# Optimization experiments

Hardware: AMD Instinct MI355X
Metric: run time of the kernel (lower is better)

## Reference

```python
import jax, jax.numpy as jnp
import numpy as np

B, T, C, H = 4, 2048, 1024, 16
D = C // H  # head dim = 64


def setup_inputs() -> dict:
    key = jax.random.key(0)
    ks = jax.random.split(key, 5)
    s = 1.0 / np.sqrt(C)
    return {
        "x": jax.random.normal(ks[0], (B, T, C), jnp.float32),
        "Wq": jax.random.normal(ks[1], (C, C), jnp.float32) * s,
        "bq": jnp.zeros((C,), jnp.float32),
        "Wk": jax.random.normal(ks[2], (C, C), jnp.float32) * s,
        "bk": jnp.zeros((C,), jnp.float32),
        "Wv": jax.random.normal(ks[3], (C, C), jnp.float32) * s,
        "bv": jnp.zeros((C,), jnp.float32),
        "Wp": jax.random.normal(ks[4], (C, C), jnp.float32) * s,
        "bp": jnp.zeros((C,), jnp.float32),
    }


def reference(x, Wq, bq, Wk, bk, Wv, bv, Wp, bp):
    # linear projections -> [B, H, T, D]
    def heads(t):
        return t.reshape(B, T, H, D).transpose(0, 2, 1, 3)
    q = heads(x @ Wq.T + bq)
    k = heads(x @ Wk.T + bk)
    v = heads(x @ Wv.T + bv)
    scale = 1.0 / np.sqrt(D)
    att = jnp.einsum("bhtd,bhsd->bhts", q, k) * scale  # [B,H,T,T]
    causal = jnp.tril(jnp.ones((T, T), bool))
    att = jnp.where(causal[None, None], att, -jnp.inf)
    att = jax.nn.softmax(att, axis=-1)
    y = jnp.einsum("bhts,bhsd->bhtd", att, v)  # [B,H,T,D]
    y = y.transpose(0, 2, 1, 3).reshape(B, T, C)
    return y @ Wp.T + bp
```

## Files before the change

### kernel.cpp

```cpp
#include <hip/hip_runtime.h>

typedef float f32x4 __attribute__((ext_vector_type(4)));
typedef float f32x16 __attribute__((ext_vector_type(16)));
typedef __bf16 bf16x8 __attribute__((ext_vector_type(8)));
typedef unsigned short u16x8 __attribute__((ext_vector_type(8)));
typedef unsigned int u32x4 __attribute__((ext_vector_type(4)));

#define SCQ 0.1803368801111183f

__device__ inline unsigned short f2bf(float f) {
  unsigned int u = __builtin_bit_cast(unsigned int, f);
  u += 0x7FFFu + ((u >> 16) & 1u);
  return (unsigned short)(u >> 16);
}

__device__ inline float fexp2(float x) {
#if __has_builtin(__builtin_amdgcn_exp2f)
  return __builtin_amdgcn_exp2f(x);
#else
  return exp2f(x);
#endif
}

__device__ inline unsigned int cvtpk_bf16(float a, float b) {
  unsigned int r;
  __asm__("v_cvt_pk_bf16_f32 %0, %1, %2" : "=v"(r) : "v"(a), "v"(b));
  return r;
}
__device__ inline void permswap32(unsigned int& a, unsigned int& b) {
  __asm__("v_permlane32_swap_b32 %0, %1" : "+v"(a), "+v"(b));
}

__device__ inline void gload_lds16(const unsigned short* g, unsigned short* l) {
  __builtin_amdgcn_global_load_lds(
      (const __attribute__((address_space(1))) unsigned int*)g,
      (__attribute__((address_space(3))) unsigned int*)l, 16, 0, 0);
}

__global__ void cvt_all(const float* __restrict__ x,
                        const float* __restrict__ wq, const float* __restrict__ wk,
                        const float* __restrict__ wv, const float* __restrict__ wp,
                        unsigned short* __restrict__ xb,
                        unsigned short* __restrict__ oq, unsigned short* __restrict__ ok,
                        unsigned short* __restrict__ ov, unsigned short* __restrict__ op_) {
  int gid = blockIdx.x;
  const float* src;
  unsigned short* dst;
  int i;
  if (gid < 8192) {
    src = x; dst = xb;
    i = (gid * 256 + threadIdx.x) * 4;
  } else {
    int g = gid - 8192;
    int m = g >> 10;
    src = (m == 0) ? wq : (m == 1) ? wk : (m == 2) ? wv : wp;
    dst = (m == 0) ? oq : (m == 1) ? ok : (m == 2) ? ov : op_;
    i = ((g & 1023) * 256 + threadIdx.x) * 4;
  }
  float4 f = *(const float4*)(src + i);
  ushort4 o;
  o.x = f2bf(f.x); o.y = f2bf(f.y); o.z = f2bf(f.z); o.w = f2bf(f.w);
  *(ushort4*)(dst + i) = o;
}

template <int MODE>
__global__ __launch_bounds__(256) void gemm128(const unsigned short* __restrict__ A,
                                               const unsigned short* __restrict__ Bt,
                                               const float* __restrict__ b0,
                                               const float* __restrict__ b1,
                                               const float* __restrict__ b2,
                                               void* __restrict__ out,
                                               unsigned short* __restrict__ vt,
                                               int M, int N, int K) {
  __shared__ __align__(16) unsigned short Sh[2][128 * 64];
  unsigned short* As = Sh[0];
  unsigned short* Bs = Sh[1];
  const int tid = threadIdx.x;
  const int lane = tid & 63, w = tid >> 6;
  const int l31 = lane & 31, half = lane >> 5;
  const int wm = w & 1, wn = w >> 1;
  const int m0 = blockIdx.x * 128, n0 = blockIdx.y * 128;

  f32x16 acc[2][2] = {};

  for (int kb = 0; kb < K; kb += 64) {
#pragma unroll
    for (int j = 0; j < 4; j++) {
      int ch = j * 256 + w * 64 + lane;
      int row = ch >> 3, pc = ch & 7;
      int c = pc ^ (row & 7);
      gload_lds16(A + (size_t)(m0 + row) * K + kb + c * 8, As + (size_t)(j * 256 + w * 64) * 8);
      gload_lds16(Bt + (size_t)(n0 + row) * K + kb + c * 8, Bs + (size_t)(j * 256 + w * 64) * 8);
    }
    __syncthreads();
#pragma unroll
    for (int ks = 0; ks < 64; ks += 16) {
      bf16x8 af[2], bfr[2];
#pragma unroll
      for (int at = 0; at < 2; at++) {
        int row = wm * 64 + at * 32 + l31;
        int pc = ((ks >> 3) + half) ^ (row & 7);
        af[at] = *(const bf16x8*)(As + row * 64 + pc * 8);
      }
#pragma unroll
      for (int nt = 0; nt < 2; nt++) {
        int row = wn * 64 + nt * 32 + l31;
        int pc = ((ks >> 3) + half) ^ (row & 7);
        bfr[nt] = *(const bf16x8*)(Bs + row * 64 + pc * 8);
      }
#pragma unroll
      for (int at = 0; at < 2; at++)
#pragma unroll
        for (int nt = 0; nt < 2; nt++)
          acc[at][nt] = __builtin_amdgcn_mfma_f32_32x32x16_bf16(af[at], bfr[nt], acc[at][nt], 0, 0, 0);
    }
    __syncthreads();
  }

  if (MODE == 0 && n0 >= 2048) {
    unsigned short* Lt = &Sh[0][0];
#pragma unroll
    for (int at = 0; at < 2; at++)
#pragma unroll
      for (int nt = 0; nt < 2; nt++) {
        int d = wn * 64 + nt * 32 + l31;
        float bv = b2[(n0 & 1023) + d];
        int swz = (d & 31) << 2;
#pragma unroll
        for (int reg = 0; reg < 16; reg++) {
          int t = wm * 64 + at * 32 + (reg & 3) + 8 * (reg >> 2) + 4 * half;
          Lt[d * 128 + (t ^ swz)] = f2bf(acc[at][nt][reg] + bv);
        }
      }
    __syncthreads();
    const int bb = m0 >> 11, t0 = m0 & 2047;
#pragma unroll
    for (int i = 0; i < 16; i++) {
      int d = (tid >> 5) + i * 8;
      int tb = (tid & 31) * 4;
      ushort4 val = *(const ushort4*)&Lt[d * 128 + (tb ^ ((d & 31) << 2))];
      int h = ((n0 & 1023) + d) >> 6;
      *(ushort4*)(vt + ((size_t)((bb * 16 + h) * 64 + (d & 63))) * 2048 + t0 + tb) = val;
    }
    return;
  }

#pragma unroll
  for (int at = 0; at < 2; at++)
#pragma unroll
    for (int nt = 0; nt < 2; nt++) {
      int col = n0 + wn * 64 + nt * 32 + l31;
      float bv, sc;
      int which = 0, cl = col;
      if (MODE == 0) {
        which = col >> 10; cl = col & 1023;
        const float* bp = (which == 0) ? b0 : b1;
        bv = bp[cl];
        sc = (which == 0) ? SCQ : 1.f;
      } else {
        bv = b0[col]; sc = 1.f;
      }
#pragma unroll
      for (int reg = 0; reg < 16; reg++) {
        int row = m0 + wm * 64 + at * 32 + (reg & 3) + 8 * (reg >> 2) + 4 * half;
        float v = (acc[at][nt][reg] + bv) * sc;
        if (MODE == 0) {
          int h = cl >> 6, d = cl & 63;
          int b = row >> 11, t = row & 2047;
          ((unsigned short*)out)[(size_t)which * 8388608 +
                                 ((size_t)((b * 16 + h) * 2048 + t)) * 64 + d] = f2bf(v);
        } else {
          ((float*)out)[(size_t)row * N + col] = v;
        }
      }
    }
}

template <int MODE>
__global__ __launch_bounds__(512, 2) void gemm8p(const unsigned short* __restrict__ A,
                                                 const unsigned short* __restrict__ Bt,
                                                 const float* __restrict__ b0,
                                                 const float* __restrict__ b1,
                                                 const float* __restrict__ b2,
                                                 void* __restrict__ out,
                                                 int M, int N, int K) {
  __shared__ __align__(16) unsigned short Lg[2][3][128 * 64];
  const int tid = threadIdx.x;
  const int lane = tid & 63, w = tid >> 6;
  const int qm = w >> 2, qn = w & 3;
  const int l15 = lane & 15, kq = lane >> 4;
  const int m0 = blockIdx.x * 128, n0 = blockIdx.y * 256;
  const int NT = K >> 6;

  const int row0 = tid >> 3, c0 = (tid & 7) ^ (row0 & 7);
  const int row1 = row0 + 64, c1 = (tid & 7) ^ (row1 & 7);

  auto stage = [&](int tt, int h) {
    if (tt < NT) {
      const unsigned short* s_ = (h == 0) ? A : Bt;
      const int rbase = (h == 0) ? m0 : (h == 1 ? n0 : n0 + 128);
      unsigned short* d = &Lg[tt & 1][h][0];
      gload_lds16(s_ + (size_t)(rbase + row0) * K + tt * 64 + c0 * 8, d + (size_t)tid * 8);
      gload_lds16(s_ + (size_t)(rbase + row1) * K + tt * 64 + c1 * 8, d + (size_t)(tid + 512) * 8);
    }
  };

  auto rdA = [&](const unsigned short* R, u16x8 (&a)[4][2]) {
#pragma unroll
    for (int mf = 0; mf < 4; mf++) {
      int row = qm * 64 + mf * 16 + l15;
#pragma unroll
      for (int kf = 0; kf < 2; kf++) {
        int pc = (kf * 4 + kq) ^ (row & 7);
        a[mf][kf] = *(const u16x8*)(R + row * 64 + pc * 8);
      }
    }
  };
  auto rdB = [&](const unsigned short* R, u16x8 (&bb)[2][2]) {
#pragma unroll
    for (int nf = 0; nf < 2; nf++) {
      int row = qn * 32 + nf * 16 + l15;
#pragma unroll
      for (int kf = 0; kf < 2; kf++) {
        int pc = (kf * 4 + kq) ^ (row & 7);
        bb[nf][kf] = *(const u16x8*)(R + row * 64 + pc * 8);
      }
    }
  };

  f32x4 acc[4][4] = {};

  auto domfma = [&](u16x8 (&a)[4][2], u16x8 (&bb)[2][2], int hb) {
#pragma unroll
    for (int mf = 0; mf < 4; mf++)
#pragma unroll
      for (int nf = 0; nf < 2; nf++)
#pragma unroll
        for (int kf = 0; kf < 2; kf++)
          acc[mf][hb * 2 + nf] = __builtin_amdgcn_mfma_f32_16x16x32_bf16(
              __builtin_bit_cast(bf16x8, a[mf][kf]),
              __builtin_bit_cast(bf16x8, bb[nf][kf]), acc[mf][hb * 2 + nf], 0, 0, 0);
  };

  stage(0, 0); stage(0, 1); stage(0, 2); stage(1, 0); stage(1, 1);
  __asm__ __volatile__("s_waitcnt vmcnt(4)" ::: "memory");
  __builtin_amdgcn_s_barrier();

  for (int tt = 0; tt < NT; ++tt) {
    const unsigned short* Ar  = &Lg[tt & 1][0][0];
    const unsigned short* B0r = &Lg[tt & 1][1][0];
    const unsigned short* B1r = &Lg[tt & 1][2][0];
    u16x8 aA[4][2], bb[2][2];

    rdA(Ar, aA); rdB(B0r, bb);
    stage(tt + 1, 2);
    __builtin_amdgcn_s_barrier();
    __asm__ __volatile__("s_waitcnt lgkmcnt(0)" ::: "memory");
    __builtin_amdgcn_sched_barrier(0);
    __builtin_amdgcn_s_setprio(1);
    domfma(aA, bb, 0);
    __builtin_amdgcn_s_setprio(0);
    __builtin_amdgcn_s_barrier();

    rdB(B1r, bb);
    stage(tt + 2, 0); stage(tt + 2, 1);
    __builtin_amdgcn_s_barrier();
    __asm__ __volatile__("s_waitcnt lgkmcnt(0)" ::: "memory");
    __builtin_amdgcn_sched_barrier(0);
    __builtin_amdgcn_s_setprio(1);
    domfma(aA, bb, 1);
    __builtin_amdgcn_s_setprio(0);
    if (tt < NT - 2) {
      __asm__ __volatile__("s_waitcnt vmcnt(4)" ::: "memory");
    } else if (tt == NT - 2) {
      __asm__ __volatile__("s_waitcnt vmcnt(0)" ::: "memory");
    }
    __builtin_amdgcn_s_barrier();
  }

#pragma unroll
  for (int nfg = 0; nfg < 4; nfg++) {
    const int col = n0 + (nfg >> 1) * 128 + qn * 32 + (nfg & 1) * 16 + l15;
    float bv = b0[col];
#pragma unroll
    for (int mf = 0; mf < 4; mf++) {
      f32x4 v4 = acc[mf][nfg];
#pragma unroll
      for (int r = 0; r < 4; r++) {
        int row = m0 + qm * 64 + mf * 16 + kq * 4 + r;
        ((float*)out)[(size_t)row * N + col] = v4[r] + bv;
      }
    }
  }
}

__global__ __launch_bounds__(256, 2) void attn_kernel(const unsigned short* __restrict__ Q,
                                                      const unsigned short* __restrict__ Km,
                                                      const unsigned short* __restrict__ Vt,
                                                      unsigned short* __restrict__ Y) {
  constexpr int T = 2048, D = 64;
  __shared__ __align__(16) unsigned short Ks[2][64 * 64];
  __shared__ __align__(16) unsigned short Vs[2][64 * 64];
  const int tid = threadIdx.x;
  const int lane = tid & 63, w = tid >> 6;
  const int l31 = lane & 31, half = lane >> 5;
  const int bh = blockIdx.x;
  const int b = bh >> 4, h = bh & 15;
  const int p = blockIdx.y;
  const unsigned short* Qp = Q + (size_t)bh * T * D;
  const unsigned short* Kp = Km + (size_t)bh * T * D;
  const unsigned short* Vp = Vt + (size_t)bh * D * T;

  const int bch0 = (w * 2) * 64, bch1 = (w * 2 + 1) * 64;
  const int ch0 = bch0 + lane, ch1 = bch1 + lane;
  const int row0 = ch0 >> 3, c0 = (ch0 & 7) ^ (row0 & 7);
  const int row1 = ch1 >> 3, c1 = (ch1 & 7) ^ (row1 & 7);

  for (int phase = 0; phase < 2; ++phase) {
    const int jt = phase ? (63 - (p * 4 + w)) : (p * 4 + w);
    const int qt = jt * 32;
    const int nit = phase ? (32 - 2 * p) : (2 * p + 2);
    const int qg = qt + l31;

    bf16x8 aq[4];
#pragma unroll
    for (int kc = 0; kc < 4; kc++)
      aq[kc] = *(const bf16x8*)(Qp + (size_t)qg * D + kc * 16 + half * 8);
    __asm__ __volatile__("" :: "v"(__builtin_bit_cast(f32x4, aq[0])),
                              "v"(__builtin_bit_cast(f32x4, aq[1])),
                              "v"(__builtin_bit_cast(f32x4, aq[2])),
                              "v"(__builtin_bit_cast(f32x4, aq[3])));

    f32x16 o0 = {}, o1 = {};
    float lsum = 0.f;

    gload_lds16(Kp + (size_t)row0 * 64 + c0 * 8, Ks[0] + bch0 * 8);
    gload_lds16(Kp + (size_t)row1 * 64 + c1 * 8, Ks[0] + bch1 * 8);
    gload_lds16(Vp + (size_t)row0 * T + c0 * 8, Vs[0] + bch0 * 8);
    gload_lds16(Vp + (size_t)row1 * T + c1 * 8, Vs[0] + bch1 * 8);

    int cur = 0;
    for (int it = 0; it < nit; ++it) {
      const int s0 = it * 64;
      if (it + 1 < nit) {
        const int s1 = s0 + 64;
        unsigned short* kd = Ks[cur ^ 1];
        unsigned short* vd = Vs[cur ^ 1];
        gload_lds16(Kp + (size_t)(s1 + row0) * 64 + c0 * 8, kd + bch0 * 8);
        gload_lds16(Kp + (size_t)(s1 + row1) * 64 + c1 * 8, kd + bch1 * 8);
        gload_lds16(Vp + (size_t)row0 * T + s1 + c0 * 8, vd + bch0 * 8);
        gload_lds16(Vp + (size_t)row1 * T + s1 + c1 * 8, vd + bch1 * 8);
        __asm__ __volatile__("s_waitcnt vmcnt(4)" ::: "memory");
      } else {
        __asm__ __volatile__("s_waitcnt vmcnt(0)" ::: "memory");
      }
      __builtin_amdgcn_s_barrier();
      __builtin_amdgcn_sched_barrier(0);

      if (s0 <= qt + 31) {
        const unsigned short* Kb_ = Ks[cur];
        const unsigned short* Vb_ = Vs[cur];

        f32x16 sacc0 = {}, sacc1 = {};
#pragma unroll
        for (int kc = 0; kc < 4; kc++) {
          int kr0 = l31;
          int cc0 = (kc * 2 + half) ^ (kr0 & 7);
          u16x8 k0 = *(const u16x8*)(Kb_ + kr0 * 64 + cc0 * 8);
          sacc0 = __builtin_amdgcn_mfma_f32_32x32x16_bf16(
              __builtin_bit_cast(bf16x8, k0), aq[kc], sacc0, 0, 0, 0);
          int kr1 = 32 + l31;
          int cc1 = (kc * 2 + half) ^ (kr1 & 7);
          u16x8 k1 = *(const u16x8*)(Kb_ + kr1 * 64 + cc1 * 8);
          sacc1 = __builtin_amdgcn_mfma_f32_32x32x16_bf16(
              __builtin_bit_cast(bf16x8, k1), aq[kc], sacc1, 0, 0, 0);
        }

        const bool full = (s0 + 63) <= qt;
        float e0_[16], e1_[16];
        if (full) {
#pragma unroll
          for (int r = 0; r < 16; r++) { e0_[r] = fexp2(sacc0[r]); lsum += e0_[r]; }
#pragma unroll
          for (int r = 0; r < 16; r++) { e1_[r] = fexp2(sacc1[r]); lsum += e1_[r]; }
        } else {
#pragma unroll
          for (int r = 0; r < 16; r++) {
            int sg = s0 + (r & 3) + 8 * (r >> 2) + 4 * half;
            float ex = fexp2(sacc0[r]);
            ex = (sg > qg) ? 0.f : ex;
            e0_[r] = ex; lsum += ex;
          }
#pragma unroll
          for (int r = 0; r < 16; r++) {
            int sg = s0 + 32 + (r & 3) + 8 * (r >> 2) + 4 * half;
            float ex = fexp2(sacc1[r]);
            ex = (sg > qg) ? 0.f : ex;
            e1_[r] = ex; lsum += ex;
          }
        }

        bf16x8 pf[4];
        auto pack2 = [&](const float* e_, int kbase) {
#pragma unroll
          for (int kl = 0; kl < 2; kl++) {
            int base = kl * 8;
            unsigned int a0 = cvtpk_bf16(e_[base + 0], e_[base + 1]);
            unsigned int b0v = cvtpk_bf16(e_[base + 4], e_[base + 5]);
            permswap32(a0, b0v);
            unsigned int a1 = cvtpk_bf16(e_[base + 2], e_[base + 3]);
            unsigned int b1v = cvtpk_bf16(e_[base + 6], e_[base + 7]);
            permswap32(a1, b1v);
            u32x4 t = {a0, a1, b0v, b1v};
            pf[kbase + kl] = __builtin_bit_cast(bf16x8, t);
          }
        };
        pack2(e0_, 0);
        pack2(e1_, 2);

#pragma unroll
        for (int kc = 0; kc < 4; kc++) {
          int vr0 = l31;
          int cc0 = (kc * 2 + half) ^ (vr0 & 7);
          u16x8 v0 = *(const u16x8*)(Vb_ + vr0 * 64 + cc0 * 8);
          o0 = __builtin_amdgcn_mfma_f32_32x32x16_bf16(
              __builtin_bit_cast(bf16x8, v0), pf[kc], o0, 0, 0, 0);
          int vr1 = 32 + l31;
          int cc1 = (kc * 2 + half) ^ (vr1 & 7);
          u16x8 v1 = *(const u16x8*)(Vb_ + vr1 * 64 + cc1 * 8);
          o1 = __builtin_amdgcn_mfma_f32_32x32x16_bf16(
              __builtin_bit_cast(bf16x8, v1), pf[kc], o1, 0, 0, 0);
        }
      }

      __builtin_amdgcn_sched_barrier(0);
      __builtin_amdgcn_s_barrier();
      cur ^= 1;
    }

    float tot = lsum + __shfl_xor(lsum, 32);
    float inv = 1.f / tot;
    unsigned short* Yrow = Y + ((size_t)(b * T + qg)) * 1024 + h * 64;
#pragma unroll
    for (int rp = 0; rp < 8; rp++) {
      int r = rp * 2;
      int d = (r & 3) + 8 * (r >> 2) + 4 * half;
      *(unsigned int*)(Yrow + d)      = cvtpk_bf16(o0[r] * inv, o0[r + 1] * inv);
      *(unsigned int*)(Yrow + 32 + d) = cvtpk_bf16(o1[r] * inv, o1[r + 1] * inv);
    }
  }
}

extern "C" void kernel_launch(void* const* d_in, const int* in_sizes, int n_in,
                              void* d_out, int out_size, void* d_ws, size_t ws_size,
                              hipStream_t stream) {
  const float* x  = (const float*)d_in[0];
  const float* Wq = (const float*)d_in[1];
  const float* bq = (const float*)d_in[2];
  const float* Wk = (const float*)d_in[3];
  const float* bk = (const float*)d_in[4];
  const float* Wv = (const float*)d_in[5];
  const float* bv = (const float*)d_in[6];
  const float* Wp = (const float*)d_in[7];
  const float* bp = (const float*)d_in[8];

  char* ws = (char*)d_ws;
  unsigned short* xb  = (unsigned short*)(ws + 0);
  unsigned short* wqb = (unsigned short*)(ws + 16777216);
  unsigned short* wkb = (unsigned short*)(ws + 18874368);
  unsigned short* wvb = (unsigned short*)(ws + 20971520);
  unsigned short* wpb = (unsigned short*)(ws + 23068672);
  unsigned short* Qb  = (unsigned short*)(ws + 25165824);
  unsigned short* Kb  = (unsigned short*)(ws + 41943040);
  unsigned short* Vtb = (unsigned short*)(ws + 58720256);
  unsigned short* Yb  = xb;

  cvt_all<<<12288, 256, 0, stream>>>(x, Wq, Wk, Wv, Wp, xb, wqb, wkb, wvb, wpb);

  gemm128<0><<<dim3(64, 24), 256, 0, stream>>>(xb, wqb, bq, bk, bv, Qb, Vtb, 8192, 3072, 1024);

  attn_kernel<<<dim3(64, 8), 256, 0, stream>>>(Qb, Kb, Vtb, Yb);

  gemm8p<1><<<dim3(64, 4), 512, 0, stream>>>(Yb, wpb, bp, bp, bp, d_out, 8192, 1024, 1024);
}
```

Before: 236.8 us.

## Replace QKV GEMM with 256x256-tile 8-wave pipelined kernel

The 128x128 single-buffered QKV projection GEMM is replaced with a 256x256-tile, 512-thread kernel. It double-buffers LDS through async global-to-LDS loads staged in quarter-tiles and interleaves LDS reads, prefetch and 16x16x32 MFMA phases with barriers and s_setprio. The aim is more operand reuse per tile and load latency hidden behind MFMA work. The V-transpose epilogue is reworked for the larger tile. In exchange it uses more LDS (128KB per block) and registers, and launches fewer blocks (384 instead of 1536), which could leave CUs underfilled.

Result: no change. 241.2 us (+1.9%).

```diff
diff --git a/kernel.cpp b/kernel.cpp
--- a/kernel.cpp
+++ b/kernel.cpp
@@ -63,125 +63,205 @@
   *(ushort4*)(dst + i) = o;
 }
 
-template <int MODE>
-__global__ __launch_bounds__(256) void gemm128(const unsigned short* __restrict__ A,
-                                               const unsigned short* __restrict__ Bt,
-                                               const float* __restrict__ b0,
-                                               const float* __restrict__ b1,
-                                               const float* __restrict__ b2,
-                                               void* __restrict__ out,
-                                               unsigned short* __restrict__ vt,
-                                               int M, int N, int K) {
-  __shared__ __align__(16) unsigned short Sh[2][128 * 64];
-  unsigned short* As = Sh[0];
-  unsigned short* Bs = Sh[1];
+__global__ __launch_bounds__(512, 2) void gemm256qkv(const unsigned short* __restrict__ A,
+                                                     const unsigned short* __restrict__ Bt,
+                                                     const float* __restrict__ b0,
+                                                     const float* __restrict__ b1,
+                                                     const float* __restrict__ b2,
+                                                     unsigned short* __restrict__ out,
+                                                     unsigned short* __restrict__ vt,
+                                                     int K) {
+  __shared__ __align__(16) unsigned short Lg[2][4][128 * 64];
   const int tid = threadIdx.x;
   const int lane = tid & 63, w = tid >> 6;
-  const int l31 = lane & 31, half = lane >> 5;
-  const int wm = w & 1, wn = w >> 1;
-  const int m0 = blockIdx.x * 128, n0 = blockIdx.y * 128;
-
-  f32x16 acc[2][2] = {};
-
-  for (int kb = 0; kb < K; kb += 64) {
-#pragma unroll
-    for (int j = 0; j < 4; j++) {
-      int ch = j * 256 + w * 64 + lane;
-      int row = ch >> 3, pc = ch & 7;
-      int c = pc ^ (row & 7);
-      gload_lds16(A + (size_t)(m0 + row) * K + kb + c * 8, As + (size_t)(j * 256 + w * 64) * 8);
-      gload_lds16(Bt + (size_t)(n0 + row) * K + kb + c * 8, Bs + (size_t)(j * 256 + w * 64) * 8);
-    }
-    __syncthreads();
-#pragma unroll
-    for (int ks = 0; ks < 64; ks += 16) {
-      bf16x8 af[2], bfr[2];
-#pragma unroll
-      for (int at = 0; at < 2; at++) {
-        int row = wm * 64 + at * 32 + l31;
-        int pc = ((ks >> 3) + half) ^ (row & 7);
-        af[at] = *(const bf16x8*)(As + row * 64 + pc * 8);
-      }
-#pragma unroll
-      for (int nt = 0; nt < 2; nt++) {
-        int row = wn * 64 + nt * 32 + l31;
-        int pc = ((ks >> 3) + half) ^ (row & 7);
-        bfr[nt] = *(const bf16x8*)(Bs + row * 64 + pc * 8);
-      }
-#pragma unroll
-      for (int at = 0; at < 2; at++)
-#pragma unroll
-        for (int nt = 0; nt < 2; nt++)
-          acc[at][nt] = __builtin_amdgcn_mfma_f32_32x32x16_bf16(af[at], bfr[nt], acc[at][nt], 0, 0, 0);
-    }
-    __syncthreads();
-  }
-
-  if (MODE == 0 && n0 >= 2048) {
-    unsigned short* Lt = &Sh[0][0];
-#pragma unroll
-    for (int at = 0; at < 2; at++)
-#pragma unroll
-      for (int nt = 0; nt < 2; nt++) {
-        int d = wn * 64 + nt * 32 + l31;
-        float bv = b2[(n0 & 1023) + d];
-        int swz = (d & 31) << 2;
-#pragma unroll
-        for (int reg = 0; reg < 16; reg++) {
-          int t = wm * 64 + at * 32 + (reg & 3) + 8 * (reg >> 2) + 4 * half;
-          Lt[d * 128 + (t ^ swz)] = f2bf(acc[at][nt][reg] + bv);
+  const int qm = w >> 2, qn = w & 3;
+  const int l15 = lane & 15, kq = lane >> 4;
+
+  const int wg = blockIdx.x;
+  const int bm = wg & 31, bn = wg >> 5;
+  const int m0 = bm * 256, n0 = bn * 256;
+  const int NT = K >> 6, NT4 = NT << 2;
+
+  const int row0 = tid >> 3, c0 = (tid & 7) ^ (row0 & 7);
+  const int row1 = row0 + 64, c1 = (tid & 7) ^ (row1 & 7);
+  const int ch0 = tid, ch1 = tid + 512;
+
+  auto stage = [&](int g) {
+    if (g < NT4) {
+      const int tt = g >> 2, h = g & 3;
+      const unsigned short* s_;
+      int rbase, reg_;
+      if (h == 0)      { s_ = A;  rbase = m0;       reg_ = 0; }
+      else if (h == 3) { s_ = A;  rbase = m0 + 128; reg_ = 1; }
+      else if (h == 1) { s_ = Bt; rbase = n0;       reg_ = 2; }
+      else             { s_ = Bt; rbase = n0 + 128; reg_ = 3; }
+      unsigned short* d = &Lg[tt & 1][reg_][0];
+      gload_lds16(s_ + (size_t)(rbase + row0) * K + tt * 64 + c0 * 8, d + ch0 * 8);
+      gload_lds16(s_ + (size_t)(rbase + row1) * K + tt * 64 + c1 * 8, d + ch1 * 8);
+    }
+  };
+
+  auto rdAh = [&](const unsigned short* R, u16x8 (&a)[4][2]) {
+#pragma unroll
+    for (int mf = 0; mf < 4; mf++) {
+      int row = qm * 64 + mf * 16 + l15;
+#pragma unroll
+      for (int kf = 0; kf < 2; kf++) {
+        int pc = (kf * 4 + kq) ^ (row & 7);
+        a[mf][kf] = *(const u16x8*)(R + row * 64 + pc * 8);
+      }
+    }
+  };
+  auto rdBh = [&](const unsigned short* R, u16x8 (&bb)[2][2]) {
+#pragma unroll
+    for (int nf = 0; nf < 2; nf++) {
+      int row = qn * 32 + nf * 16 + l15;
+#pragma unroll
+      for (int kf = 0; kf < 2; kf++) {
+        int pc = (kf * 4 + kq) ^ (row & 7);
+        bb[nf][kf] = *(const u16x8*)(R + row * 64 + pc * 8);
+      }
+    }
+  };
+  auto domfma = [&](u16x8 (&a)[4][2], u16x8 (&bb)[2][2], f32x4 (*ac)[2]) {
+#pragma unroll
+    for (int mf = 0; mf < 4; mf++)
+#pragma unroll
+      for (int nf = 0; nf < 2; nf++)
+#pragma unroll
+        for (int kf = 0; kf < 2; kf++)
+          ac[mf][nf] = __builtin_amdgcn_mfma_f32_16x16x32_bf16(
+              __builtin_bit_cast(bf16x8, a[mf][kf]),
+              __builtin_bit_cast(bf16x8, bb[nf][kf]), ac[mf][nf], 0, 0, 0);
+  };
+
+  f32x4 acc[4][4][2] = {};
+
+#pragma unroll
+  for (int g = 0; g < 7; ++g) stage(g);
+  __asm__ __volatile__("s_waitcnt vmcnt(6)" ::: "memory");
+  __builtin_amdgcn_s_barrier();
+
+  for (int tt = 0; tt < NT; ++tt) {
+    const unsigned short* A0r = &Lg[tt & 1][0][0];
+    const unsigned short* A1r = &Lg[tt & 1][1][0];
+    const unsigned short* B0r = &Lg[tt & 1][2][0];
+    const unsigned short* B1r = &Lg[tt & 1][3][0];
+    const int gb = 7 + 4 * tt;
+    u16x8 aA[4][2], bb0[2][2], bb1[2][2];
+
+    rdAh(A0r, aA); rdBh(B0r, bb0);
+    stage(gb + 0);
+    __builtin_amdgcn_s_barrier();
+    __asm__ __volatile__("s_waitcnt lgkmcnt(0)" ::: "memory");
+    __builtin_amdgcn_sched_barrier(0);
+    __builtin_amdgcn_s_setprio(1);
+    domfma(aA, bb0, acc[0]);
+    __builtin_amdgcn_s_setprio(0);
+    __builtin_amdgcn_s_barrier();
+
+    rdBh(B1r, bb1);
+    stage(gb + 1);
+    __builtin_amdgcn_s_barrier();
+    __asm__ __volatile__("s_waitcnt lgkmcnt(0)" ::: "memory");
+    __builtin_amdgcn_sched_barrier(0);
+    __builtin_amdgcn_s_setprio(1);
+    domfma(aA, bb1, acc[1]);
+    __builtin_amdgcn_s_setprio(0);
+    __builtin_amdgcn_s_barrier();
+
+    rdAh(A1r, aA);
+    stage(gb + 2);
+    __builtin_amdgcn_s_barrier();
+    __asm__ __volatile__("s_waitcnt lgkmcnt(0)" ::: "memory");
+    __builtin_amdgcn_sched_barrier(0);
+    __builtin_amdgcn_s_setprio(1);
+    domfma(aA, bb0, acc[2]);
+    __builtin_amdgcn_s_setprio(0);
+    __builtin_amdgcn_s_barrier();
+
+    stage(gb + 3);
+    __builtin_amdgcn_s_setprio(1);
+    domfma(aA, bb1, acc[3]);
+    __builtin_amdgcn_s_setprio(0);
+    if (tt < NT - 2) {
+      __asm__ __volatile__("s_waitcnt vmcnt(6)" ::: "memory");
+    } else if (tt == NT - 2) {
+      __asm__ __volatile__("s_waitcnt vmcnt(0)" ::: "memory");
+    }
+    __builtin_amdgcn_s_barrier();
+  }
+
+  if (n0 >= 2048) {
+    unsigned short* Ld = &Lg[0][0][0];
+    const int bb_ = m0 >> 11, t0g = m0 & 2047;
+    const int vbase = n0 - 2048;
+#pragma unroll
+    for (int dh = 0; dh < 2; dh++) {
+      if (dh) __syncthreads();
+#pragma unroll
+      for (int ph = 0; ph < 2; ph++) {
+        const int p = ph * 2 + dh;
+#pragma unroll
+        for (int nf = 0; nf < 2; nf++) {
+          const int dl = qn * 32 + nf * 16 + l15;
+          const float bv = b2[vbase + dh * 128 + dl];
+          const int swz = (dl & 31) << 2;
+#pragma unroll
+          for (int mf = 0; mf < 4; mf++) {
+            f32x4 v4 = acc[p][mf][nf];
+#pragma unroll
+            for (int rp = 0; rp < 2; rp++) {
+              const int tl = ph * 128 + qm * 64 + mf * 16 + kq * 4 + rp * 2;
+              unsigned int pk = cvtpk_bf16(v4[rp * 2] + bv, v4[rp * 2 + 1] + bv);
+              *(unsigned int*)&Ld[dl * 256 + (tl ^ swz)] = pk;
+            }
+          }
         }
       }
-    __syncthreads();
-    const int bb = m0 >> 11, t0 = m0 & 2047;
-#pragma unroll
-    for (int i = 0; i < 16; i++) {
-      int d = (tid >> 5) + i * 8;
-      int tb = (tid & 31) * 4;
-      ushort4 val = *(const ushort4*)&Lt[d * 128 + (tb ^ ((d & 31) << 2))];
-      int h = ((n0 & 1023) + d) >> 6;
-      *(ushort4*)(vt + ((size_t)((bb * 16 + h) * 64 + (d & 63))) * 2048 + t0 + tb) = val;
+      __syncthreads();
+#pragma unroll
+      for (int i = 0; i < 16; i++) {
+        const int d = (tid >> 5) + (i & 7) * 16;
+        const int tb = (tid & 31) * 4 + (i >> 3) * 128;
+        ushort4 val = *(const ushort4*)&Ld[d * 256 + (tb ^ ((d & 31) << 2))];
+        const int cl = vbase + dh * 128 + d;
+        const int hh = cl >> 6, dd = cl & 63;
+        *(ushort4*)(vt + ((size_t)((bb_ * 16 + hh) * 64 + dd)) * 2048 + t0g + tb) = val;
+      }
     }
     return;
   }
 
 #pragma unroll
-  for (int at = 0; at < 2; at++)
-#pragma unroll
-    for (int nt = 0; nt < 2; nt++) {
-      int col = n0 + wn * 64 + nt * 32 + l31;
-      float bv, sc;
-      int which = 0, cl = col;
-      if (MODE == 0) {
-        which = col >> 10; cl = col & 1023;
-        const float* bp = (which == 0) ? b0 : b1;
-        bv = bp[cl];
-        sc = (which == 0) ? SCQ : 1.f;
-      } else {
-        bv = b0[col]; sc = 1.f;
-      }
-#pragma unroll
-      for (int reg = 0; reg < 16; reg++) {
-        int row = m0 + wm * 64 + at * 32 + (reg & 3) + 8 * (reg >> 2) + 4 * half;
-        float v = (acc[at][nt][reg] + bv) * sc;
-        if (MODE == 0) {
-          int h = cl >> 6, d = cl & 63;
+  for (int p = 0; p < 4; p++) {
+    const int rb = m0 + (p >> 1) * 128 + qm * 64 + kq * 4;
+    const int cb = n0 + (p & 1) * 128 + qn * 32 + l15;
+#pragma unroll
+    for (int nf = 0; nf < 2; nf++) {
+      const int col = cb + nf * 16;
+      const int which = col >> 10, cl = col & 1023;
+      const float bv = (which == 0) ? b0[cl] : b1[cl];
+      const float sc = (which == 0) ? SCQ : 1.f;
+      const int hh = cl >> 6, dd = cl & 63;
+#pragma unroll
+      for (int mf = 0; mf < 4; mf++) {
+        f32x4 v4 = acc[p][mf][nf];
+#pragma unroll
+        for (int r = 0; r < 4; r++) {
+          int row = rb + mf * 16 + r;
           int b = row >> 11, t = row & 2047;
-          ((unsigned short*)out)[(size_t)which * 8388608 +
-                                 ((size_t)((b * 16 + h) * 2048 + t)) * 64 + d] = f2bf(v);
-        } else {
-          ((float*)out)[(size_t)row * N + col] = v;
+          out[(size_t)which * 8388608 +
+              ((size_t)((b * 16 + hh) * 2048 + t)) * 64 + dd] = f2bf((v4[r] + bv) * sc);
         }
       }
     }
-}
-
-template <int MODE>
+  }
+}
+
 __global__ __launch_bounds__(512, 2) void gemm8p(const unsigned short* __restrict__ A,
                                                  const unsigned short* __restrict__ Bt,
                                                  const float* __restrict__ b0,
-                                                 const float* __restrict__ b1,
-                                                 const float* __restrict__ b2,
                                                  void* __restrict__ out,
                                                  int M, int N, int K) {
   __shared__ __align__(16) unsigned short Lg[2][3][128 * 64];
@@ -477,9 +557,9 @@
 
   cvt_all<<<12288, 256, 0, stream>>>(x, Wq, Wk, Wv, Wp, xb, wqb, wkb, wvb, wpb);
 
-  gemm128<0><<<dim3(64, 24), 256, 0, stream>>>(xb, wqb, bq, bk, bv, Qb, Vtb, 8192, 3072, 1024);
+  gemm256qkv<<<384, 512, 0, stream>>>(xb, wqb, bq, bk, bv, Qb, Vtb, 1024);
 
   attn_kernel<<<dim3(64, 8), 256, 0, stream>>>(Qb, Kb, Vtb, Yb);
 
-  gemm8p<1><<<dim3(64, 4), 512, 0, stream>>>(Yb, wpb, bp, bp, bp, d_out, 8192, 1024, 1024);
-}
+  gemm8p<<<dim3(64, 4), 512, 0, stream>>>(Yb, wpb, bp, d_out, 8192, 1024, 1024);
+}
```
